# Performance work log

Measured on AMD Instinct MI355X. Metric: run time of the kernel, lower is better.

Reference implementation:

```python
import jax, jax.numpy as jnp
import numpy as np

N, E, D, H, C, G = 50000, 800000, 128, 128, 10, 128


def _xavier(key, shape):
    fan_out, fan_in = shape
    a = float(np.sqrt(6.0 / (fan_in + fan_out)))
    return jax.random.uniform(key, shape, jnp.float32, -a, a)


def setup_inputs() -> dict:
    key = jax.random.key(0)
    ks = jax.random.split(key, 10)
    x = jax.random.normal(ks[0], (N, D), jnp.float32)
    edge_index = jax.random.randint(ks[1], (2, E), 0, N, dtype=jnp.int64) if jax.config.jax_enable_x64 else jax.random.randint(ks[1], (2, E), 0, N, dtype=jnp.int32)
    batch = jnp.sort(jax.random.randint(ks[2], (N,), 0, G, dtype=jnp.int32))
    return {
        "x": x,
        "edge_index": edge_index,
        "batch": batch,
        "W1_rel": _xavier(ks[3], (H, D)),
        "b1": jnp.zeros((H,), jnp.float32),
        "W1_root": _xavier(ks[4], (H, D)),
        "W2": _xavier(ks[5], (H, H)),
        "b2": jnp.zeros((H,), jnp.float32),
        "W3": _xavier(ks[6], (H, H)),
        "b3": jnp.zeros((H,), jnp.float32),
        "Wl": _xavier(ks[7], (C, H)),
        "bl": jnp.zeros((C,), jnp.float32),
    }


def reference(x, edge_index, batch, W1_rel, b1, W1_root, W2, b2, W3, b3, Wl, bl):
    n = x.shape[0]
    row, col = edge_index[0], edge_index[1]

    # conv1: PyG GraphConv(aggr='add'): lin_rel(sum_j x_j) + lin_root(x)
    agg = jax.ops.segment_sum(x[row], col, num_segments=n)  # [N, D]
    h = agg @ W1_rel.T + b1 + x @ W1_root.T
    h = jax.nn.relu(h)

    # self-loops + symmetric degree norm (shared by conv2/conv3)
    sl = jnp.arange(n, dtype=row.dtype)
    row2 = jnp.concatenate([row, sl])
    col2 = jnp.concatenate([col, sl])
    deg = jax.ops.segment_sum(jnp.ones_like(col2, x.dtype), col2, num_segments=n)
    dinv = jnp.where(deg > 0, deg ** -0.5, 0.0)
    norm = dinv[row2] * dinv[col2]  # [E+N]

    def gcn(hin, W, b):
        hp = hin @ W.T                      # [N, H]
        msg = hp[row2] * norm[:, None]      # gather + per-edge scale
        return jax.ops.segment_sum(msg, col2, num_segments=n) + b

    h = jax.nn.relu(gcn(h, W2, b2))
    h = gcn(h, W3, b3)

    # global mean pool over graphs
    sums = jax.ops.segment_sum(h, batch, num_segments=G)
    cnt = jax.ops.segment_sum(jnp.ones_like(batch, h.dtype), batch, num_segments=G)
    pooled = sums / jnp.maximum(cnt, 1.0)[:, None]

    # F.normalize(p=2, dim=1) with eps=1e-12
    xn = pooled / jnp.maximum(jnp.linalg.norm(pooled, axis=1, keepdims=True), 1e-12)
    Wn = Wl / jnp.maximum(jnp.linalg.norm(Wl, axis=1, keepdims=True), 1e-12)
    out = xn @ Wn.T + bl  # dropout inactive in eval mode
    return (xn, out)
```

## Files before the change

kernel.cpp:

```cpp
#include <hip/hip_runtime.h>

#define HID 128

typedef __attribute__((ext_vector_type(8))) short short8;
typedef __attribute__((ext_vector_type(4))) float f32x4;

__device__ inline ushort f2b(float f) {
    union { float f; uint u; } v; v.f = f;
    uint u = v.u;
    return (ushort)((u + 0x7fffu + ((u >> 16) & 1u)) >> 16);
}

__device__ inline void fma8(float* acc, uint4 u, float s) {
    acc[0] += __uint_as_float(u.x << 16) * s;
    acc[1] += __uint_as_float(u.x & 0xffff0000u) * s;
    acc[2] += __uint_as_float(u.y << 16) * s;
    acc[3] += __uint_as_float(u.y & 0xffff0000u) * s;
    acc[4] += __uint_as_float(u.z << 16) * s;
    acc[5] += __uint_as_float(u.z & 0xffff0000u) * s;
    acc[6] += __uint_as_float(u.w << 16) * s;
    acc[7] += __uint_as_float(u.w & 0xffff0000u) * s;
}

__global__ __launch_bounds__(256) void gc_deg_count(const int* __restrict__ col,
                                                    int* __restrict__ deg, int E) {
    int e = blockIdx.x * 256 + threadIdx.x;
    if (e < E) atomicAdd(&deg[col[e]], 1);
}

__global__ __launch_bounds__(256) void gc_scan_part(const int* __restrict__ deg,
                                                    int* __restrict__ bsum, int n) {
    __shared__ int s[4];
    int i = blockIdx.x * 256 + threadIdx.x;
    int v = (i < n) ? deg[i] : 0;
#pragma unroll
    for (int off = 32; off >= 1; off >>= 1) v += __shfl_xor(v, off, 64);
    if ((threadIdx.x & 63) == 0) s[threadIdx.x >> 6] = v;
    __syncthreads();
    if (threadIdx.x == 0) bsum[blockIdx.x] = s[0] + s[1] + s[2] + s[3];
}

__global__ __launch_bounds__(256) void gc_scan_top(int* __restrict__ bsum, int B) {
    __shared__ int s[256];
    int t = threadIdx.x;
    int v = (t < B) ? bsum[t] : 0;
    s[t] = v;
    __syncthreads();
    for (int off = 1; off < 256; off <<= 1) {
        int u = (t >= off) ? s[t - off] : 0;
        __syncthreads();
        s[t] += u;
        __syncthreads();
    }
    int excl = (t == 0) ? 0 : s[t - 1];
    if (t < B) bsum[t] = excl;
}

__global__ __launch_bounds__(256) void gc_scan_final(const int* __restrict__ deg,
                                                     const int* __restrict__ bsum,
                                                     int* __restrict__ offs,
                                                     int* __restrict__ curs,
                                                     float* __restrict__ dinv, int n) {
    __shared__ int s[256];
    int t = threadIdx.x;
    int i = blockIdx.x * 256 + t;
    int v = (i < n) ? deg[i] : 0;
    s[t] = v;
    __syncthreads();
    for (int off = 1; off < 256; off <<= 1) {
        int u = (t >= off) ? s[t - off] : 0;
        __syncthreads();
        s[t] += u;
        __syncthreads();
    }
    int excl = ((t == 0) ? 0 : s[t - 1]) + bsum[blockIdx.x];
    if (i < n) {
        offs[i] = excl;
        curs[i] = excl;
        dinv[i] = rsqrtf((float)v + 1.0f);
        if (i == n - 1) offs[n] = excl + v;
    }
}

__global__ __launch_bounds__(256) void gc_fill_xcd(const int* __restrict__ row,
                                                   const int* __restrict__ col,
                                                   int* __restrict__ cursor,
                                                   ushort* __restrict__ eid,
                                                   int E, float pscale) {
    const int part = blockIdx.x & 7;
    int e = (blockIdx.x >> 3) * 256 + threadIdx.x;
    if (e >= E) return;
    int c = col[e];
    int p = min(7, (int)((float)c * pscale));
    if (p != part) return;
    int pos = atomicAdd(&cursor[c], 1);
    eid[pos] = (ushort)row[e];
}

__global__ __launch_bounds__(256) void gc_cvt_all(const float* __restrict__ x,
                                                  const float* __restrict__ Wa,
                                                  const float* __restrict__ Wb,
                                                  const float* __restrict__ Wc,
                                                  const float* __restrict__ Wd,
                                                  ushort* __restrict__ xb,
                                                  ushort* __restrict__ wb, int n8x) {
    int i = blockIdx.x * 256 + threadIdx.x;
    const float* src;
    ushort* dst;
    int off;
    if (i < n8x) {
        src = x; dst = xb; off = i;
    } else {
        int k = i - n8x;
        if (k >= 8192) return;
        int seg = k >> 11;
        off = k & 2047;
        src = (seg == 0) ? Wa : (seg == 1) ? Wb : (seg == 2) ? Wc : Wd;
        dst = wb + (size_t)seg * 16384;
    }
    const float4* s4 = (const float4*)src;
    float4 a = s4[off * 2], b = s4[off * 2 + 1];
    uint4 o;
    o.x = (uint)f2b(a.x) | ((uint)f2b(a.y) << 16);
    o.y = (uint)f2b(a.z) | ((uint)f2b(a.w) << 16);
    o.z = (uint)f2b(b.x) | ((uint)f2b(b.y) << 16);
    o.w = (uint)f2b(b.z) | ((uint)f2b(b.w) << 16);
    ((uint4*)dst)[off] = o;
}

__global__ __launch_bounds__(256) void gc_gather_b(const int* __restrict__ offs,
                                                   const ushort* __restrict__ eid,
                                                   const ushort* __restrict__ src,
                                                   const float* __restrict__ dinv,
                                                   const ushort* __restrict__ selfh,
                                                   const float* __restrict__ bias,
                                                   ushort* __restrict__ dst,
                                                   int n, int do_relu) {
    int node = (blockIdx.x * 256 + threadIdx.x) >> 4;
    if (node >= n) return;
    const int c = threadIdx.x & 15;
    const int s = offs[node], e = offs[node + 1];
    const bool un = (dinv != nullptr);
    const float dd = un ? dinv[node] : 1.0f;
    const uint4* __restrict__ src4 = (const uint4*)src;

    float acc[8];
#pragma unroll
    for (int k = 0; k < 8; ++k) acc[k] = 0.f;

    int j = s;
    for (; j + 7 < e; j += 8) {
        int r[8];
        float sc[8];
        uint4 u[8];
#pragma unroll
        for (int k = 0; k < 8; ++k) r[k] = eid[j + k];
#pragma unroll
        for (int k = 0; k < 8; ++k) sc[k] = un ? dinv[r[k]] * dd : 1.0f;
#pragma unroll
        for (int k = 0; k < 8; ++k) u[k] = src4[(size_t)r[k] * 16 + c];
#pragma unroll
        for (int k = 0; k < 8; ++k) fma8(acc, u[k], sc[k]);
    }
    for (; j + 3 < e; j += 4) {
        int r[4];
        float sc[4];
        uint4 u[4];
#pragma unroll
        for (int k = 0; k < 4; ++k) r[k] = eid[j + k];
#pragma unroll
        for (int k = 0; k < 4; ++k) sc[k] = un ? dinv[r[k]] * dd : 1.0f;
#pragma unroll
        for (int k = 0; k < 4; ++k) u[k] = src4[(size_t)r[k] * 16 + c];
#pragma unroll
        for (int k = 0; k < 4; ++k) fma8(acc, u[k], sc[k]);
    }
    for (; j < e; ++j) {
        int r0 = eid[j];
        float s0 = un ? dinv[r0] * dd : 1.0f;
        fma8(acc, src4[(size_t)r0 * 16 + c], s0);
    }
    if (selfh) {
        float di2 = dd * dd;
        fma8(acc, ((const uint4*)selfh)[(size_t)node * 16 + c], di2);
#pragma unroll
        for (int k = 0; k < 8; ++k) acc[k] += bias[c * 8 + k];
    }
    if (do_relu) {
#pragma unroll
        for (int k = 0; k < 8; ++k) acc[k] = fmaxf(acc[k], 0.f);
    }
    uint4 o;
    o.x = (uint)f2b(acc[0]) | ((uint)f2b(acc[1]) << 16);
    o.y = (uint)f2b(acc[2]) | ((uint)f2b(acc[3]) << 16);
    o.z = (uint)f2b(acc[4]) | ((uint)f2b(acc[5]) << 16);
    o.w = (uint)f2b(acc[6]) | ((uint)f2b(acc[7]) << 16);
    ((uint4*)dst)[(size_t)node * 16 + c] = o;
}

__global__ __launch_bounds__(256) void gc_gemm_mfma(const ushort* __restrict__ A1,
                                                    const ushort* __restrict__ W1,
                                                    const ushort* __restrict__ A2,
                                                    const ushort* __restrict__ W2,
                                                    const float* __restrict__ bias,
                                                    ushort* __restrict__ out,
                                                    int nrows, int do_relu) {
    __shared__ ushort lds[128 * 136];
    const int t = threadIdx.x;
    const int w = t >> 6;
    const int l = t & 63;
    const int lr = l & 15;
    const int g = l >> 4;
    const int row0 = blockIdx.x * 64 + w * 16;

    f32x4 acc[8];
#pragma unroll
    for (int i = 0; i < 8; ++i) acc[i] = (f32x4){0.f, 0.f, 0.f, 0.f};

    const int nmat = (A2 != nullptr) ? 2 : 1;
    for (int mat = 0; mat < nmat; ++mat) {
        const ushort* __restrict__ A = mat ? A2 : A1;
        const ushort* __restrict__ W = mat ? W2 : W1;
        __syncthreads();
#pragma unroll
        for (int i = 0; i < 8; ++i) {
            int cid = i * 256 + t;
            int r = cid >> 4, ch = cid & 15;
            *(uint4*)(&lds[r * 136 + ch * 8]) = ((const uint4*)W)[cid];
        }
        __syncthreads();

        short8 af[4];
        const int arow = row0 + lr;
        const bool ok = arow < nrows;
#pragma unroll
        for (int ks = 0; ks < 4; ++ks) {
            if (ok)
                af[ks] = *(const short8*)(A + (size_t)arow * 128 + ks * 32 + g * 8);
            else
                af[ks] = (short8){0, 0, 0, 0, 0, 0, 0, 0};
        }
#pragma unroll
        for (int ct = 0; ct < 8; ++ct) {
#pragma unroll
            for (int ks = 0; ks < 4; ++ks) {
                short8 bf = *(const short8*)(&lds[(ct * 16 + lr) * 136 + ks * 32 + g * 8]);
                acc[ct] = __builtin_amdgcn_mfma_f32_16x16x32_bf16(af[ks], bf, acc[ct], 0, 0, 0);
            }
        }
    }

    float bv[8];
#pragma unroll
    for (int ct = 0; ct < 8; ++ct) bv[ct] = bias ? bias[ct * 16 + lr] : 0.f;

    __syncthreads();
    ushort* ep = &lds[w * (16 * 136)];
#pragma unroll
    for (int ct = 0; ct < 8; ++ct) {
#pragma unroll
        for (int r = 0; r < 4; ++r) {
            float v = acc[ct][r] + bv[ct];
            if (do_relu) v = fmaxf(v, 0.f);
            ep[(g * 4 + r) * 136 + ct * 16 + lr] = f2b(v);
        }
    }
    __syncthreads();
#pragma unroll
    for (int i = 0; i < 4; ++i) {
        int rr = i * 4 + g;
        int grow = row0 + rr;
        if (grow < nrows) {
            uint4 vv = *(uint4*)(&ep[rr * 136 + lr * 8]);
            ((uint4*)out)[(size_t)grow * 16 + lr] = vv;
        }
    }
}

__global__ __launch_bounds__(256) void gc_pool(const ushort* __restrict__ h,
                                               const int* __restrict__ batch,
                                               float* __restrict__ psum,
                                               float* __restrict__ pcnt, int n) {
    int base = blockIdx.x * 128;
    int sub = threadIdx.x >> 6;
    int fp = threadIdx.x & 63;
    int start = base + sub * 32;
    int end = min(start + 32, n);
    if (start >= end) return;
    int cur = batch[start];
    float s0 = 0.f, s1 = 0.f;
    int run = 0;
    const uint* h2 = (const uint*)h;
    for (int node = start; node < end; ++node) {
        int g = batch[node];
        if (g != cur) {
            unsafeAtomicAdd(&psum[cur * HID + fp * 2 + 0], s0);
            unsafeAtomicAdd(&psum[cur * HID + fp * 2 + 1], s1);
            if (fp == 0) unsafeAtomicAdd(&pcnt[cur], (float)run);
            s0 = s1 = 0.f; run = 0; cur = g;
        }
        uint u = h2[(size_t)node * 64 + fp];
        s0 += __uint_as_float(u << 16);
        s1 += __uint_as_float(u & 0xffff0000u);
        ++run;
    }
    unsafeAtomicAdd(&psum[cur * HID + fp * 2 + 0], s0);
    unsafeAtomicAdd(&psum[cur * HID + fp * 2 + 1], s1);
    if (fp == 0) unsafeAtomicAdd(&pcnt[cur], (float)run);
}

__global__ __launch_bounds__(128) void gc_finalize(const float* __restrict__ psum,
                                                   const float* __restrict__ pcnt,
                                                   const float* __restrict__ Wl,
                                                   const float* __restrict__ bl,
                                                   float* __restrict__ xn,
                                                   float* __restrict__ outp, int C) {
    int g = blockIdx.x;
    int f = threadIdx.x;
    __shared__ float xrow[128];
    __shared__ float s2[2];
    float cn = fmaxf(pcnt[g], 1.0f);
    float v = psum[g * HID + f] / cn;
    float ss = v * v;
#pragma unroll
    for (int off = 32; off >= 1; off >>= 1) ss += __shfl_xor(ss, off, 64);
    if ((f & 63) == 0) s2[f >> 6] = ss;
    __syncthreads();
    float denom = fmaxf(sqrtf(s2[0] + s2[1]), 1e-12f);
    float xv = v / denom;
    xn[g * HID + f] = xv;
    xrow[f] = xv;
    __syncthreads();
    if (f < 64) {
        for (int cc = 0; cc < C; ++cc) {
            float w0 = Wl[cc * HID + 2 * f + 0];
            float w1 = Wl[cc * HID + 2 * f + 1];
            float nrm = w0 * w0 + w1 * w1;
            float dot = xrow[2 * f] * w0 + xrow[2 * f + 1] * w1;
#pragma unroll
            for (int off = 32; off >= 1; off >>= 1) {
                nrm += __shfl_xor(nrm, off, 64);
                dot += __shfl_xor(dot, off, 64);
            }
            if (f == 0) outp[g * C + cc] = dot / fmaxf(sqrtf(nrm), 1e-12f) + bl[cc];
        }
    }
}

extern "C" void kernel_launch(void* const* d_in, const int* in_sizes, int n_in,
                              void* d_out, int out_size, void* d_ws, size_t ws_size,
                              hipStream_t stream) {
    const float* x      = (const float*)d_in[0];
    const int*   ei     = (const int*)d_in[1];
    const int*   batch  = (const int*)d_in[2];
    const float* W1_rel = (const float*)d_in[3];
    const float* b1     = (const float*)d_in[4];
    const float* W1_root= (const float*)d_in[5];
    const float* W2     = (const float*)d_in[6];
    const float* b2     = (const float*)d_in[7];
    const float* W3     = (const float*)d_in[8];
    const float* b3     = (const float*)d_in[9];
    const float* Wl     = (const float*)d_in[10];
    const float* bl     = (const float*)d_in[11];

    const int N = in_sizes[0] / HID;
    const int E = in_sizes[1] / 2;
    const int C = 10;
    const int G = out_size / (HID + C);

    const int* row = ei;
    const int* col = ei + E;

    ushort* xb  = (ushort*)d_ws;
    ushort* hb0 = xb  + (size_t)N * HID;
    ushort* hb1 = hb0 + (size_t)N * HID;
    ushort* wb  = hb1 + (size_t)N * HID;
    float* dinv = (float*)(wb + 4 * 16384);
    float* psum = dinv + N;
    float* pcnt = psum + (size_t)G * HID;
    int*   degi = (int*)(pcnt + G);
    int*   offs = degi + N;
    int*   curs = offs + N + 1;
    ushort* eid = (ushort*)(curs + N);
    int*   bsum = (int*)(eid + ((E + 1) & ~1));

    float* xn   = (float*)d_out;
    float* outp = xn + (size_t)G * HID;

    const int eb256 = (E + 255) / 256;
    const int nb256 = (N + 255) / 256;
    const int gthb  = (N * 16 + 255) / 256;
    const int gmb   = (N + 63) / 64;
    const float pscale = 8.0f / (float)N;
    const int n8x   = N * HID / 8;
    const int cvb   = (n8x + 8192 + 255) / 256;

    hipMemsetAsync(psum, 0, ((size_t)G * HID + G + N) * sizeof(float), stream);

    gc_deg_count<<<eb256, 256, 0, stream>>>(col, degi, E);
    gc_scan_part<<<nb256, 256, 0, stream>>>(degi, bsum, N);
    gc_scan_top<<<1, 256, 0, stream>>>(bsum, nb256);
    gc_scan_final<<<nb256, 256, 0, stream>>>(degi, bsum, offs, curs, dinv, N);
    gc_fill_xcd<<<eb256 * 8, 256, 0, stream>>>(row, col, curs, eid, E, pscale);

    gc_cvt_all<<<cvb, 256, 0, stream>>>(x, W1_rel, W1_root, W2, W3, xb, wb, n8x);

    gc_gather_b<<<gthb, 256, 0, stream>>>(offs, eid, xb, nullptr, nullptr, nullptr, hb0, N, 0);
    gc_gemm_mfma<<<gmb, 256, 0, stream>>>(hb0, wb, xb, wb + 16384, b1, hb1, N, 1);

    gc_gemm_mfma<<<gmb, 256, 0, stream>>>(hb1, wb + 2 * 16384, nullptr, nullptr, nullptr, hb0, N, 0);
    gc_gather_b<<<gthb, 256, 0, stream>>>(offs, eid, hb0, dinv, hb0, b2, hb1, N, 1);

    gc_gemm_mfma<<<gmb, 256, 0, stream>>>(hb1, wb + 3 * 16384, nullptr, nullptr, nullptr, hb0, N, 0);
    gc_gather_b<<<gthb, 256, 0, stream>>>(offs, eid, hb0, dinv, hb0, b3, hb1, N, 0);

    gc_pool<<<(N + 127) / 128, 256, 0, stream>>>(hb1, batch, psum, pcnt, N);
    gc_finalize<<<G, 128, 0, stream>>>(psum, pcnt, Wl, bl, xn, outp, C);
}
```

Baseline: 339.3 us.

## Fuse neighbor aggregation and MFMA transform into one kernel per conv layer

Replaces the separate gather and GEMM kernels with a single kernel per layer. Each block aggregates neighbor features for 64 nodes into LDS, then multiplies by the weight matrix with MFMA, reading weights directly from global memory. For the GCN layers this reorders the work to aggregate first and transform second, which is mathematically equivalent because both steps are linear. The aim is to cut intermediate bf16 writes and reads plus kernel launches. In exchange, each thread now serially gathers four nodes and far fewer blocks are launched, which reduces latency hiding in the gather phase.

Measured after the change: 452.9 us. 33.5% more time.

```diff
diff --git a/kernel.cpp b/kernel.cpp
--- a/kernel.cpp
+++ b/kernel.cpp
@@ -128,131 +128,120 @@
     ((uint4*)dst)[off] = o;
 }
 
-__global__ __launch_bounds__(256) void gc_gather_b(const int* __restrict__ offs,
-                                                   const ushort* __restrict__ eid,
-                                                   const ushort* __restrict__ src,
-                                                   const float* __restrict__ dinv,
-                                                   const ushort* __restrict__ selfh,
-                                                   const float* __restrict__ bias,
-                                                   ushort* __restrict__ dst,
-                                                   int n, int do_relu) {
-    int node = (blockIdx.x * 256 + threadIdx.x) >> 4;
-    if (node >= n) return;
-    const int c = threadIdx.x & 15;
-    const int s = offs[node], e = offs[node + 1];
-    const bool un = (dinv != nullptr);
-    const float dd = un ? dinv[node] : 1.0f;
+__global__ __launch_bounds__(256) void gc_conv_fused(const int* __restrict__ offs,
+                                                     const ushort* __restrict__ eid,
+                                                     const ushort* __restrict__ src,
+                                                     const float* __restrict__ dinv,
+                                                     const ushort* __restrict__ root,
+                                                     const ushort* __restrict__ W,
+                                                     const ushort* __restrict__ Wroot,
+                                                     const float* __restrict__ bias,
+                                                     ushort* __restrict__ out,
+                                                     int n, int do_relu) {
+    __shared__ ushort lds[64 * 136];
+    const int t = threadIdx.x;
+    const int node0 = blockIdx.x * 64;
     const uint4* __restrict__ src4 = (const uint4*)src;
 
-    float acc[8];
-#pragma unroll
-    for (int k = 0; k < 8; ++k) acc[k] = 0.f;
-
-    int j = s;
-    for (; j + 7 < e; j += 8) {
-        int r[8];
-        float sc[8];
-        uint4 u[8];
-#pragma unroll
-        for (int k = 0; k < 8; ++k) r[k] = eid[j + k];
-#pragma unroll
-        for (int k = 0; k < 8; ++k) sc[k] = un ? dinv[r[k]] * dd : 1.0f;
-#pragma unroll
-        for (int k = 0; k < 8; ++k) u[k] = src4[(size_t)r[k] * 16 + c];
-#pragma unroll
-        for (int k = 0; k < 8; ++k) fma8(acc, u[k], sc[k]);
-    }
-    for (; j + 3 < e; j += 4) {
-        int r[4];
-        float sc[4];
-        uint4 u[4];
-#pragma unroll
-        for (int k = 0; k < 4; ++k) r[k] = eid[j + k];
-#pragma unroll
-        for (int k = 0; k < 4; ++k) sc[k] = un ? dinv[r[k]] * dd : 1.0f;
-#pragma unroll
-        for (int k = 0; k < 4; ++k) u[k] = src4[(size_t)r[k] * 16 + c];
-#pragma unroll
-        for (int k = 0; k < 4; ++k) fma8(acc, u[k], sc[k]);
-    }
-    for (; j < e; ++j) {
-        int r0 = eid[j];
-        float s0 = un ? dinv[r0] * dd : 1.0f;
-        fma8(acc, src4[(size_t)r0 * 16 + c], s0);
-    }
-    if (selfh) {
-        float di2 = dd * dd;
-        fma8(acc, ((const uint4*)selfh)[(size_t)node * 16 + c], di2);
-#pragma unroll
-        for (int k = 0; k < 8; ++k) acc[k] += bias[c * 8 + k];
-    }
-    if (do_relu) {
-#pragma unroll
-        for (int k = 0; k < 8; ++k) acc[k] = fmaxf(acc[k], 0.f);
-    }
-    uint4 o;
-    o.x = (uint)f2b(acc[0]) | ((uint)f2b(acc[1]) << 16);
-    o.y = (uint)f2b(acc[2]) | ((uint)f2b(acc[3]) << 16);
-    o.z = (uint)f2b(acc[4]) | ((uint)f2b(acc[5]) << 16);
-    o.w = (uint)f2b(acc[6]) | ((uint)f2b(acc[7]) << 16);
-    ((uint4*)dst)[(size_t)node * 16 + c] = o;
-}
-
-__global__ __launch_bounds__(256) void gc_gemm_mfma(const ushort* __restrict__ A1,
-                                                    const ushort* __restrict__ W1,
-                                                    const ushort* __restrict__ A2,
-                                                    const ushort* __restrict__ W2,
-                                                    const float* __restrict__ bias,
-                                                    ushort* __restrict__ out,
-                                                    int nrows, int do_relu) {
-    __shared__ ushort lds[128 * 136];
-    const int t = threadIdx.x;
+    {
+        const int qw = t >> 4;
+        const int c = t & 15;
+        const bool un = (dinv != nullptr);
+#pragma unroll
+        for (int ni = 0; ni < 4; ++ni) {
+            int lrow = ni * 16 + qw;
+            int node = node0 + lrow;
+            float acc[8];
+#pragma unroll
+            for (int k = 0; k < 8; ++k) acc[k] = 0.f;
+            if (node < n) {
+                const int s = offs[node], e = offs[node + 1];
+                const float dd = un ? dinv[node] : 1.0f;
+                int j = s;
+                for (; j + 7 < e; j += 8) {
+                    int r[8]; float sc[8]; uint4 u[8];
+#pragma unroll
+                    for (int k = 0; k < 8; ++k) r[k] = eid[j + k];
+#pragma unroll
+                    for (int k = 0; k < 8; ++k) sc[k] = un ? dinv[r[k]] * dd : 1.0f;
+#pragma unroll
+                    for (int k = 0; k < 8; ++k) u[k] = src4[(size_t)r[k] * 16 + c];
+#pragma unroll
+                    for (int k = 0; k < 8; ++k) fma8(acc, u[k], sc[k]);
+                }
+                for (; j + 3 < e; j += 4) {
+                    int r[4]; float sc[4]; uint4 u[4];
+#pragma unroll
+                    for (int k = 0; k < 4; ++k) r[k] = eid[j + k];
+#pragma unroll
+                    for (int k = 0; k < 4; ++k) sc[k] = un ? dinv[r[k]] * dd : 1.0f;
+#pragma unroll
+                    for (int k = 0; k < 4; ++k) u[k] = src4[(size_t)r[k] * 16 + c];
+#pragma unroll
+                    for (int k = 0; k < 4; ++k) fma8(acc, u[k], sc[k]);
+                }
+                for (; j < e; ++j) {
+                    int r0 = eid[j];
+                    float s0 = un ? dinv[r0] * dd : 1.0f;
+                    fma8(acc, src4[(size_t)r0 * 16 + c], s0);
+                }
+                if (un) fma8(acc, src4[(size_t)node * 16 + c], dd * dd);
+            }
+            uint4 o;
+            o.x = (uint)f2b(acc[0]) | ((uint)f2b(acc[1]) << 16);
+            o.y = (uint)f2b(acc[2]) | ((uint)f2b(acc[3]) << 16);
+            o.z = (uint)f2b(acc[4]) | ((uint)f2b(acc[5]) << 16);
+            o.w = (uint)f2b(acc[6]) | ((uint)f2b(acc[7]) << 16);
+            *(uint4*)(&lds[lrow * 136 + c * 8]) = o;
+        }
+    }
+    __syncthreads();
+
     const int w = t >> 6;
     const int l = t & 63;
     const int lr = l & 15;
     const int g = l >> 4;
-    const int row0 = blockIdx.x * 64 + w * 16;
 
     f32x4 acc[8];
 #pragma unroll
     for (int i = 0; i < 8; ++i) acc[i] = (f32x4){0.f, 0.f, 0.f, 0.f};
 
-    const int nmat = (A2 != nullptr) ? 2 : 1;
-    for (int mat = 0; mat < nmat; ++mat) {
-        const ushort* __restrict__ A = mat ? A2 : A1;
-        const ushort* __restrict__ W = mat ? W2 : W1;
-        __syncthreads();
-#pragma unroll
-        for (int i = 0; i < 8; ++i) {
-            int cid = i * 256 + t;
-            int r = cid >> 4, ch = cid & 15;
-            *(uint4*)(&lds[r * 136 + ch * 8]) = ((const uint4*)W)[cid];
-        }
-        __syncthreads();
-
-        short8 af[4];
-        const int arow = row0 + lr;
-        const bool ok = arow < nrows;
+    short8 af[4];
+#pragma unroll
+    for (int ks = 0; ks < 4; ++ks)
+        af[ks] = *(const short8*)(&lds[(w * 16 + lr) * 136 + ks * 32 + g * 8]);
+#pragma unroll
+    for (int ct = 0; ct < 8; ++ct) {
+#pragma unroll
+        for (int ks = 0; ks < 4; ++ks) {
+            short8 bf = *(const short8*)(W + (size_t)(ct * 16 + lr) * 128 + ks * 32 + g * 8);
+            acc[ct] = __builtin_amdgcn_mfma_f32_16x16x32_bf16(af[ks], bf, acc[ct], 0, 0, 0);
+        }
+    }
+    if (root) {
+        const int grow = node0 + w * 16 + lr;
+        const bool ok = grow < n;
+        short8 af2[4];
 #pragma unroll
         for (int ks = 0; ks < 4; ++ks) {
             if (ok)
-                af[ks] = *(const short8*)(A + (size_t)arow * 128 + ks * 32 + g * 8);
+                af2[ks] = *(const short8*)(root + (size_t)grow * 128 + ks * 32 + g * 8);
             else
-                af[ks] = (short8){0, 0, 0, 0, 0, 0, 0, 0};
+                af2[ks] = (short8){0, 0, 0, 0, 0, 0, 0, 0};
         }
 #pragma unroll
         for (int ct = 0; ct < 8; ++ct) {
 #pragma unroll
             for (int ks = 0; ks < 4; ++ks) {
-                short8 bf = *(const short8*)(&lds[(ct * 16 + lr) * 136 + ks * 32 + g * 8]);
-                acc[ct] = __builtin_amdgcn_mfma_f32_16x16x32_bf16(af[ks], bf, acc[ct], 0, 0, 0);
+                short8 bf = *(const short8*)(Wroot + (size_t)(ct * 16 + lr) * 128 + ks * 32 + g * 8);
+                acc[ct] = __builtin_amdgcn_mfma_f32_16x16x32_bf16(af2[ks], bf, acc[ct], 0, 0, 0);
             }
         }
     }
 
     float bv[8];
 #pragma unroll
-    for (int ct = 0; ct < 8; ++ct) bv[ct] = bias ? bias[ct * 16 + lr] : 0.f;
+    for (int ct = 0; ct < 8; ++ct) bv[ct] = bias[ct * 16 + lr];
 
     __syncthreads();
     ushort* ep = &lds[w * (16 * 136)];
@@ -269,8 +258,8 @@
 #pragma unroll
     for (int i = 0; i < 4; ++i) {
         int rr = i * 4 + g;
-        int grow = row0 + rr;
-        if (grow < nrows) {
+        int grow = node0 + w * 16 + rr;
+        if (grow < n) {
             uint4 vv = *(uint4*)(&ep[rr * 136 + lr * 8]);
             ((uint4*)out)[(size_t)grow * 16 + lr] = vv;
         }
@@ -389,11 +378,9 @@
 
     const int eb256 = (E + 255) / 256;
     const int nb256 = (N + 255) / 256;
-    const int gthb  = (N * 16 + 255) / 256;
-    const int gmb   = (N + 63) / 64;
+    const int cvb   = (N * HID / 8 + 8192 + 255) / 256;
+    const int cb    = (N + 63) / 64;
     const float pscale = 8.0f / (float)N;
-    const int n8x   = N * HID / 8;
-    const int cvb   = (n8x + 8192 + 255) / 256;
 
     hipMemsetAsync(psum, 0, ((size_t)G * HID + G + N) * sizeof(float), stream);
 
@@ -403,17 +390,15 @@
     gc_scan_final<<<nb256, 256, 0, stream>>>(degi, bsum, offs, curs, dinv, N);
     gc_fill_xcd<<<eb256 * 8, 256, 0, stream>>>(row, col, curs, eid, E, pscale);
 
-    gc_cvt_all<<<cvb, 256, 0, stream>>>(x, W1_rel, W1_root, W2, W3, xb, wb, n8x);
-
-    gc_gather_b<<<gthb, 256, 0, stream>>>(offs, eid, xb, nullptr, nullptr, nullptr, hb0, N, 0);
-    gc_gemm_mfma<<<gmb, 256, 0, stream>>>(hb0, wb, xb, wb + 16384, b1, hb1, N, 1);
-
-    gc_gemm_mfma<<<gmb, 256, 0, stream>>>(hb1, wb + 2 * 16384, nullptr, nullptr, nullptr, hb0, N, 0);
-    gc_gather_b<<<gthb, 256, 0, stream>>>(offs, eid, hb0, dinv, hb0, b2, hb1, N, 1);
-
-    gc_gemm_mfma<<<gmb, 256, 0, stream>>>(hb1, wb + 3 * 16384, nullptr, nullptr, nullptr, hb0, N, 0);
-    gc_gather_b<<<gthb, 256, 0, stream>>>(offs, eid, hb0, dinv, hb0, b3, hb1, N, 0);
-
-    gc_pool<<<(N + 127) / 128, 256, 0, stream>>>(hb1, batch, psum, pcnt, N);
+    gc_cvt_all<<<cvb, 256, 0, stream>>>(x, W1_rel, W1_root, W2, W3, xb, wb, N * HID / 8);
+
+    gc_conv_fused<<<cb, 256, 0, stream>>>(offs, eid, xb, nullptr, xb,
+                                          wb, wb + 16384, b1, hb0, N, 1);
+    gc_conv_fused<<<cb, 256, 0, stream>>>(offs, eid, hb0, dinv, nullptr,
+                                          wb + 2 * 16384, nullptr, b2, hb1, N, 1);
+    gc_conv_fused<<<cb, 256, 0, stream>>>(offs, eid, hb1, dinv, nullptr,
+                                          wb + 3 * 16384, nullptr, b3, hb0, N, 0);
+
+    gc_pool<<<(N + 127) / 128, 256, 0, stream>>>(hb0, batch, psum, pcnt, N);
     gc_finalize<<<G, 128, 0, stream>>>(psum, pcnt, Wl, bl, xn, outp, C);
 }
```
